# Optimization experiments

Measured on AMD Instinct MI355X. Metric: run time of the kernel, lower is better.

The kernel has to match this reference:

```python
import jax, jax.numpy as jnp
import numpy as np

MODES = 2
LC = 4
N = 6000
KNN = 10
NODES = 64
CH = MODES ** 2
M = N * 2 * (KNN + 1)  # total candidate couplings


def setup_inputs() -> dict:
    key = jax.random.key(0)
    ks = jax.random.split(key, 6)
    return {
        "CK_inputs": jax.random.normal(ks[0], (N, 2 * (KNN + 1), 3), dtype=jnp.float32),
        "W_in": jax.random.normal(ks[1], (3, NODES), dtype=jnp.float32) * 0.1,
        "b_in": jnp.zeros((NODES,), dtype=jnp.float32),
        "W_hid": jax.random.normal(ks[2], (LC - 1, NODES, NODES), dtype=jnp.float32) * 0.1,
        "b_hid": jnp.zeros((LC - 1, NODES), dtype=jnp.float32),
        "W_out": jax.random.normal(ks[3], (NODES, CH), dtype=jnp.float32) * 0.1,
        "b_out": jnp.zeros((CH,), dtype=jnp.float32),
        "coo": jax.random.randint(ks[4], (2, M), 0, N, dtype=jnp.int32),
    }


def _mlp(x, W_in, b_in, W_hid, b_hid, W_out, b_out):
    # MLP: 3 -> 64, (LC-1) hidden 64->64 layers, 64 -> CH; ReLU activations.
    h = jax.nn.relu(x @ W_in + b_in)
    for i in range(W_hid.shape[0]):  # small fixed layer count
        h = jax.nn.relu(h @ W_hid[i] + b_hid[i])
    return h @ W_out + b_out  # [M, CH]


def reference(CK_inputs, W_in, b_in, W_hid, b_hid, W_out, b_out, coo):
    C_stripped = _mlp(CK_inputs.reshape(-1, 3), W_in, b_in, W_hid, b_hid, W_out, b_out)  # [M, CH]
    D = MODES * N
    # Original: for channel ch = mi*MODES+mj, scatter C_stripped[:, ch] at indices coo*MODES+mj
    # (mj added to BOTH row and col, replicating the source exactly). Indices are
    # independent of mi, so sum over mi first, then one scatter-add per mj.
    vals = C_stripped.reshape(-1, MODES, MODES).sum(axis=1)  # [M, MODES]; axis1=mi, axis2=mj
    dense = jnp.zeros((D, D), dtype=CK_inputs.dtype)
    for mj in range(MODES):
        idx = coo * MODES + mj  # [2, M]
        dense = dense.at[idx[0], idx[1]].add(vals[:, mj])
    return dense
```

## Files before the change

kernel.cpp:

```cpp
#include <hip/hip_runtime.h>
#include <stdint.h>

#define NN    6000
#define KNNC  10
#define MM    (NN * 2 * (KNNC + 1))
#define DD    (2 * NN)
#define LCH   3
#define BLK   256

#define RB        256
#define RPL       4
#define MLPGRID   ((MM + RB - 1) / RB)
#define OUTBYTES  ((size_t)DD * DD * 4)

__global__ __launch_bounds__(BLK, 2) void mlp_scatter(
    const float* __restrict__ CK,
    const float* __restrict__ Win,
    const float* __restrict__ bin,
    const float* __restrict__ Whid,
    const float* __restrict__ bhid,
    const float* __restrict__ Wout,
    const float* __restrict__ bout,
    const int* __restrict__ coo,
    float* __restrict__ out)
{
    __shared__ float sW[64 * 64];
    __shared__ float sH[64 * RB];

    const int tid   = threadIdx.x;
    const int wave  = tid >> 6;
    const int lane  = tid & 63;
    const int jo    = wave << 4;
    const int rbase = blockIdx.x * RB;
    const int mb0   = rbase + lane * 4;
    const int mb    = mb0 < MM ? mb0 : MM - 4;

    const float4 f0 = *(const float4*)(CK + mb * 3);
    const float4 f1 = *(const float4*)(CK + mb * 3 + 4);
    const float4 f2 = *(const float4*)(CK + mb * 3 + 8);
    const float x0[RPL] = {f0.x, f0.w, f1.z, f2.y};
    const float x1[RPL] = {f0.y, f1.x, f1.w, f2.z};
    const float x2[RPL] = {f0.z, f1.y, f2.x, f2.w};

#pragma unroll
    for (int jj = 0; jj < 16; jj++) {
        const int j = jo + jj;
        const float w0 = Win[j], w1 = Win[64 + j], w2 = Win[128 + j];
        const float bj = bin[j];
        float4 hv;
        hv.x = fmaxf(fmaf(x2[0], w2, fmaf(x1[0], w1, fmaf(x0[0], w0, bj))), 0.f);
        hv.y = fmaxf(fmaf(x2[1], w2, fmaf(x1[1], w1, fmaf(x0[1], w0, bj))), 0.f);
        hv.z = fmaxf(fmaf(x2[2], w2, fmaf(x1[2], w1, fmaf(x0[2], w0, bj))), 0.f);
        hv.w = fmaxf(fmaf(x2[3], w2, fmaf(x1[3], w1, fmaf(x0[3], w0, bj))), 0.f);
        *(float4*)(sH + j * RB + lane * 4) = hv;
    }
    __syncthreads();

#pragma unroll 1
    for (int l = 0; l < LCH; l++) {
        {
            const float4* __restrict__ Wg = (const float4*)(Whid + (l << 12));
            float4* __restrict__ sW4 = (float4*)sW;
#pragma unroll
            for (int i = 0; i < 4; i++) sW4[i * 256 + tid] = Wg[i * 256 + tid];
        }
        __syncthreads();

        float g[RPL][16];
#pragma unroll
        for (int jj = 0; jj < 16; jj++) {
            const float bj = bhid[(l << 6) + jo + jj];
#pragma unroll
            for (int r = 0; r < RPL; r++) g[r][jj] = bj;
        }

#pragma unroll 4
        for (int k = 0; k < 64; k++) {
            const float4 wa = *(const float4*)(sW + (k << 6) + jo);
            const float4 wb = *(const float4*)(sW + (k << 6) + jo + 4);
            const float4 wc = *(const float4*)(sW + (k << 6) + jo + 8);
            const float4 wd = *(const float4*)(sW + (k << 6) + jo + 12);
            const float4 hv = *(const float4*)(sH + k * RB + lane * 4);
            const float hk[RPL] = {hv.x, hv.y, hv.z, hv.w};
#pragma unroll
            for (int r = 0; r < RPL; r++) {
                g[r][0]  = fmaf(wa.x, hk[r], g[r][0]);
                g[r][1]  = fmaf(wa.y, hk[r], g[r][1]);
                g[r][2]  = fmaf(wa.z, hk[r], g[r][2]);
                g[r][3]  = fmaf(wa.w, hk[r], g[r][3]);
                g[r][4]  = fmaf(wb.x, hk[r], g[r][4]);
                g[r][5]  = fmaf(wb.y, hk[r], g[r][5]);
                g[r][6]  = fmaf(wb.z, hk[r], g[r][6]);
                g[r][7]  = fmaf(wb.w, hk[r], g[r][7]);
                g[r][8]  = fmaf(wc.x, hk[r], g[r][8]);
                g[r][9]  = fmaf(wc.y, hk[r], g[r][9]);
                g[r][10] = fmaf(wc.z, hk[r], g[r][10]);
                g[r][11] = fmaf(wc.w, hk[r], g[r][11]);
                g[r][12] = fmaf(wd.x, hk[r], g[r][12]);
                g[r][13] = fmaf(wd.y, hk[r], g[r][13]);
                g[r][14] = fmaf(wd.z, hk[r], g[r][14]);
                g[r][15] = fmaf(wd.w, hk[r], g[r][15]);
            }
        }
        __syncthreads();

#pragma unroll
        for (int jj = 0; jj < 16; jj++) {
            float4 hv;
            hv.x = fmaxf(g[0][jj], 0.f);
            hv.y = fmaxf(g[1][jj], 0.f);
            hv.z = fmaxf(g[2][jj], 0.f);
            hv.w = fmaxf(g[3][jj], 0.f);
            *(float4*)(sH + (jo + jj) * RB + lane * 4) = hv;
        }
        __syncthreads();
    }

    float v0[RPL], v1[RPL];
    const float b02 = bout[0] + bout[2], b13 = bout[1] + bout[3];
#pragma unroll
    for (int r = 0; r < RPL; r++) { v0[r] = b02; v1[r] = b13; }
#pragma unroll 8
    for (int k = 0; k < 64; k++) {
        const float4 wo = ((const float4*)Wout)[k];
        const float wxz = wo.x + wo.z, wyw = wo.y + wo.w;
        const float4 hv = *(const float4*)(sH + k * RB + lane * 4);
        v0[0] = fmaf(hv.x, wxz, v0[0]);  v1[0] = fmaf(hv.x, wyw, v1[0]);
        v0[1] = fmaf(hv.y, wxz, v0[1]);  v1[1] = fmaf(hv.y, wyw, v1[1]);
        v0[2] = fmaf(hv.z, wxz, v0[2]);  v1[2] = fmaf(hv.z, wyw, v1[2]);
        v0[3] = fmaf(hv.w, wxz, v0[3]);  v1[3] = fmaf(hv.w, wyw, v1[3]);
    }

    if (mb0 < MM) {
        const int mrow = mb0 + wave;
        const float sv0 = wave == 0 ? v0[0] : wave == 1 ? v0[1]
                        : wave == 2 ? v0[2] : v0[3];
        const float sv1 = wave == 0 ? v1[0] : wave == 1 ? v1[1]
                        : wave == 2 ? v1[2] : v1[3];
        const int r2 = coo[mrow] * 2;
        const int c2 = coo[MM + mrow] * 2;
        const long long f0i = (long long)r2 * DD + c2;
        unsafeAtomicAdd(out + f0i, sv0);
        unsafeAtomicAdd(out + f0i + DD + 1, sv1);
    }
}

extern "C" void kernel_launch(void* const* d_in, const int* in_sizes, int n_in,
                              void* d_out, int out_size, void* d_ws, size_t ws_size,
                              hipStream_t stream) {
    const float* CK   = (const float*)d_in[0];
    const float* Win  = (const float*)d_in[1];
    const float* bin  = (const float*)d_in[2];
    const float* Whid = (const float*)d_in[3];
    const float* bhid = (const float*)d_in[4];
    const float* Wout = (const float*)d_in[5];
    const float* bout = (const float*)d_in[6];
    const int* coo    = (const int*)d_in[7];
    float* out        = (float*)d_out;

    hipMemsetAsync(out, 0, OUTBYTES, stream);
    mlp_scatter<<<MLPGRID, BLK, 0, stream>>>(
        CK, Win, bin, Whid, bhid, Wout, bout, coo, out);
}
```

Baseline: 662.4 us.

## Halve rows per block, read hidden weights directly from global, raise occupancy

Each block now handles 128 rows with 2 rows per lane instead of 256 rows with 4, and launch bounds target 4 blocks per SM. The shared-memory staging of hidden-layer weights and its barrier are removed. Weights are read straight from global memory via a wave-uniform offset, intended to become scalar/cached loads. This cuts register and LDS pressure to improve latency hiding, at the cost of less weight reuse per load and more global traffic for the weights. The 48 MB memset of the output likely dominates total time anyway.

```diff
diff --git a/kernel.cpp b/kernel.cpp
--- a/kernel.cpp
+++ b/kernel.cpp
@@ -8,12 +8,12 @@
 #define LCH   3
 #define BLK   256
 
-#define RB        256
-#define RPL       4
+#define RB        128
+#define RPL       2
 #define MLPGRID   ((MM + RB - 1) / RB)
 #define OUTBYTES  ((size_t)DD * DD * 4)
 
-__global__ __launch_bounds__(BLK, 2) void mlp_scatter(
+__global__ __launch_bounds__(BLK, 4) void mlp_scatter(
     const float* __restrict__ CK,
     const float* __restrict__ Win,
     const float* __restrict__ bin,
@@ -24,64 +24,57 @@
     const int* __restrict__ coo,
     float* __restrict__ out)
 {
-    __shared__ float sW[64 * 64];
     __shared__ float sH[64 * RB];
 
-    const int tid   = threadIdx.x;
-    const int wave  = tid >> 6;
-    const int lane  = tid & 63;
-    const int jo    = wave << 4;
+    const int tid  = threadIdx.x;
+    const int wave = tid >> 6;
+    const int lane = tid & 63;
+    const int jo = __builtin_amdgcn_readfirstlane((tid >> 6) << 4);
+
     const int rbase = blockIdx.x * RB;
-    const int mb0   = rbase + lane * 4;
-    const int mb    = mb0 < MM ? mb0 : MM - 4;
+    const int mb0   = rbase + lane * 2;
+    const int mb    = mb0 < MM ? mb0 : MM - 2;
 
-    const float4 f0 = *(const float4*)(CK + mb * 3);
-    const float4 f1 = *(const float4*)(CK + mb * 3 + 4);
-    const float4 f2 = *(const float4*)(CK + mb * 3 + 8);
-    const float x0[RPL] = {f0.x, f0.w, f1.z, f2.y};
-    const float x1[RPL] = {f0.y, f1.x, f1.w, f2.z};
-    const float x2[RPL] = {f0.z, f1.y, f2.x, f2.w};
+    const float2 ca = *(const float2*)(CK + mb * 3);
+    const float2 cb = *(const float2*)(CK + mb * 3 + 2);
+    const float2 cc = *(const float2*)(CK + mb * 3 + 4);
+    const float x0[RPL] = {ca.x, cb.y};
+    const float x1[RPL] = {ca.y, cc.x};
+    const float x2[RPL] = {cb.x, cc.y};
 
 #pragma unroll
     for (int jj = 0; jj < 16; jj++) {
         const int j = jo + jj;
         const float w0 = Win[j], w1 = Win[64 + j], w2 = Win[128 + j];
         const float bj = bin[j];
-        float4 hv;
+        float2 hv;
         hv.x = fmaxf(fmaf(x2[0], w2, fmaf(x1[0], w1, fmaf(x0[0], w0, bj))), 0.f);
         hv.y = fmaxf(fmaf(x2[1], w2, fmaf(x1[1], w1, fmaf(x0[1], w0, bj))), 0.f);
-        hv.z = fmaxf(fmaf(x2[2], w2, fmaf(x1[2], w1, fmaf(x0[2], w0, bj))), 0.f);
-        hv.w = fmaxf(fmaf(x2[3], w2, fmaf(x1[3], w1, fmaf(x0[3], w0, bj))), 0.f);
-        *(float4*)(sH + j * RB + lane * 4) = hv;
+        *(float2*)(sH + j * RB + lane * 2) = hv;
     }
     __syncthreads();
 
 #pragma unroll 1
     for (int l = 0; l < LCH; l++) {
-        {
-            const float4* __restrict__ Wg = (const float4*)(Whid + (l << 12));
-            float4* __restrict__ sW4 = (float4*)sW;
-#pragma unroll
-            for (int i = 0; i < 4; i++) sW4[i * 256 + tid] = Wg[i * 256 + tid];
-        }
-        __syncthreads();
+        const float* __restrict__ Wl = Whid + (l << 12) + jo;
+        const float* __restrict__ bh = bhid + (l << 6) + jo;
 
         float g[RPL][16];
 #pragma unroll
         for (int jj = 0; jj < 16; jj++) {
-            const float bj = bhid[(l << 6) + jo + jj];
-#pragma unroll
-            for (int r = 0; r < RPL; r++) g[r][jj] = bj;
+            const float bj = bh[jj];
+            g[0][jj] = bj;
+            g[1][jj] = bj;
         }
 
 #pragma unroll 4
         for (int k = 0; k < 64; k++) {
-            const float4 wa = *(const float4*)(sW + (k << 6) + jo);
-            const float4 wb = *(const float4*)(sW + (k << 6) + jo + 4);
-            const float4 wc = *(const float4*)(sW + (k << 6) + jo + 8);
-            const float4 wd = *(const float4*)(sW + (k << 6) + jo + 12);
-            const float4 hv = *(const float4*)(sH + k * RB + lane * 4);
-            const float hk[RPL] = {hv.x, hv.y, hv.z, hv.w};
+            const float4 wa = *(const float4*)(Wl + (k << 6));
+            const float4 wb = *(const float4*)(Wl + (k << 6) + 4);
+            const float4 wc = *(const float4*)(Wl + (k << 6) + 8);
+            const float4 wd = *(const float4*)(Wl + (k << 6) + 12);
+            const float2 hv = *(const float2*)(sH + k * RB + lane * 2);
+            const float hk[RPL] = {hv.x, hv.y};
 #pragma unroll
             for (int r = 0; r < RPL; r++) {
                 g[r][0]  = fmaf(wa.x, hk[r], g[r][0]);
@@ -106,12 +99,10 @@
 
 #pragma unroll
         for (int jj = 0; jj < 16; jj++) {
-            float4 hv;
+            float2 hv;
             hv.x = fmaxf(g[0][jj], 0.f);
             hv.y = fmaxf(g[1][jj], 0.f);
-            hv.z = fmaxf(g[2][jj], 0.f);
-            hv.w = fmaxf(g[3][jj], 0.f);
-            *(float4*)(sH + (jo + jj) * RB + lane * 4) = hv;
+            *(float2*)(sH + (jo + jj) * RB + lane * 2) = hv;
         }
         __syncthreads();
     }
@@ -124,24 +115,22 @@
     for (int k = 0; k < 64; k++) {
         const float4 wo = ((const float4*)Wout)[k];
         const float wxz = wo.x + wo.z, wyw = wo.y + wo.w;
-        const float4 hv = *(const float4*)(sH + k * RB + lane * 4);
+        const float2 hv = *(const float2*)(sH + k * RB + lane * 2);
         v0[0] = fmaf(hv.x, wxz, v0[0]);  v1[0] = fmaf(hv.x, wyw, v1[0]);
         v0[1] = fmaf(hv.y, wxz, v0[1]);  v1[1] = fmaf(hv.y, wyw, v1[1]);
-        v0[2] = fmaf(hv.z, wxz, v0[2]);  v1[2] = fmaf(hv.z, wyw, v1[2]);
-        v0[3] = fmaf(hv.w, wxz, v0[3]);  v1[3] = fmaf(hv.w, wyw, v1[3]);
     }
 
-    if (mb0 < MM) {
+    if (wave < 2) {
         const int mrow = mb0 + wave;
-        const float sv0 = wave == 0 ? v0[0] : wave == 1 ? v0[1]
-                        : wave == 2 ? v0[2] : v0[3];
-        const float sv1 = wave == 0 ? v1[0] : wave == 1 ? v1[1]
-                        : wave == 2 ? v1[2] : v1[3];
-        const int r2 = coo[mrow] * 2;
-        const int c2 = coo[MM + mrow] * 2;
-        const long long f0i = (long long)r2 * DD + c2;
-        unsafeAtomicAdd(out + f0i, sv0);
-        unsafeAtomicAdd(out + f0i + DD + 1, sv1);
+        if (mrow < MM) {
+            const float sv0 = wave == 0 ? v0[0] : v0[1];
+            const float sv1 = wave == 0 ? v1[0] : v1[1];
+            const int r2 = coo[mrow] * 2;
+            const int c2 = coo[MM + mrow] * 2;
+            const long long f0i = (long long)r2 * DD + c2;
+            unsafeAtomicAdd(out + f0i, sv0);
+            unsafeAtomicAdd(out + f0i + DD + 1, sv1);
+        }
     }
 }
 
```

After: 649.0 us. 2.0% less time.
